# Kernel optimization log

Measured on AMD Instinct MI355X. Metric: run time of the kernel, lower is better.

Reference implementation:

```python
import jax, jax.numpy as jnp
import numpy as np
from jax import lax

B, R, F = 100, 15, 4096       # batch, regions, feature dim
V, E, D, A, T = 10000, 1024, 1024, 512, 500  # vocab, embed, decoder, attention, topic
LIN = 1024                    # autoencoder linear output width
NT = 5                        # sentences per paragraph
L = 52                        # max caption length


def setup_inputs() -> dict:
    key = jax.random.key(0)
    ks = jax.random.split(key, 16)
    g = lambda i, shp, s: jax.random.normal(ks[i], shp, jnp.float32) * s
    return {
        "image_features": g(0, (B, R, F), 1.0),
        "encoded_captions": jax.random.randint(ks[1], (B, NT, L), 0, V),
        "caption_lengths": jax.random.randint(ks[2], (B, NT), 1, L),
        # autoencoder
        "W_lt": g(3, (LIN, F), 0.02), "b_lt": jnp.zeros((LIN,), jnp.float32),
        "conv_w": g(4, (6, 1, 15, 26), 0.05), "conv_b": jnp.zeros((6,), jnp.float32),
        # attention MLP (weight_norm linears == plain linears mathematically)
        "W_feat": g(5, (A, F), 0.02), "b_feat": jnp.zeros((A,), jnp.float32),
        "W_dec": g(6, (A, D), 0.02), "b_dec": jnp.zeros((A,), jnp.float32),
        "W_top": g(7, (A, T), 0.02), "b_top": jnp.zeros((A,), jnp.float32),
        "W_full": g(8, (1, A), 0.02), "b_full": jnp.zeros((1,), jnp.float32),
        # embedding + LSTM cells + output heads
        "emb": g(9, (V, E), 0.1),
        "W_ih1": g(10, (4 * D, E + F + D), 0.01), "W_hh1": g(11, (4 * D, D), 0.01),
        "b_ih1": jnp.zeros((4 * D,), jnp.float32), "b_hh1": jnp.zeros((4 * D,), jnp.float32),
        "W_ih2": g(12, (4 * D, F + D), 0.01), "W_hh2": g(13, (4 * D, D), 0.01),
        "b_ih2": jnp.zeros((4 * D,), jnp.float32), "b_hh2": jnp.zeros((4 * D,), jnp.float32),
        "W_fc1": g(14, (V, D), 0.02), "b_fc1": jnp.zeros((V,), jnp.float32),
        "W_fc": g(15, (V, D), 0.02), "b_fc": jnp.zeros((V,), jnp.float32),
    }


def _lstm_cell(x, h, c, W_ih, W_hh, b_ih, b_hh):
    gates = x @ W_ih.T + b_ih + h @ W_hh.T + b_hh
    i, f, g_, o = jnp.split(gates, 4, axis=-1)
    c = jax.nn.sigmoid(f) * c + jax.nn.sigmoid(i) * jnp.tanh(g_)
    h = jax.nn.sigmoid(o) * jnp.tanh(c)
    return h, c


def reference(image_features, encoded_captions, caption_lengths, W_lt, b_lt,
              conv_w, conv_b, W_feat, b_feat, W_dec, b_dec, W_top, b_top,
              W_full, b_full, emb, W_ih1, W_hh1, b_ih1, b_hh1,
              W_ih2, W_hh2, b_ih2, b_hh2, W_fc1, b_fc1, W_fc, b_fc):
    def per_sample(img, caps, lens):
        # img (R,F), caps (NT,L) int, lens (NT,) int
        img_mean = img.mean(0)  # (F,)
        # autoencoder: linear 4096->1024, conv2d(1->6, k=(15,26), stride 2)
        x = (img @ W_lt.T + b_lt)[None, None]  # (1,1,R,LIN)
        conv = lax.conv_general_dilated(x, conv_w, (2, 2), "VALID",
                                        dimension_numbers=("NCHW", "OIHW", "NCHW"))
        topics = conv[0, :, 0, :] + conv_b[:, None]  # (6, T=500)
        att1 = img @ W_feat.T + b_feat               # (R,A), precomputed once
        # last word of each sentence: caps[t, lens[t]-1]
        last_words = jnp.take_along_axis(caps, (lens - 1)[:, None], axis=1)[:, 0]  # (NT,)
        last_embs = emb[last_words]                  # (NT,E)

        def step(carry, tup):
            h1, c1, h2, c2 = carry
            topic_t, emb_t = tup
            # top-down attention LSTM: cat([h2, img_mean, word_emb])
            x1 = jnp.concatenate([h2, img_mean, emb_t])
            h1, c1 = _lstm_cell(x1, h1, c1, W_ih1, W_hh1, b_ih1, b_hh1)
            # attention over R regions (dropout is identity in eval)
            att = jax.nn.relu(att1 + (h1 @ W_dec.T + b_dec) + (topic_t @ W_top.T + b_top))
            scores = att @ W_full[0] + b_full[0]     # (R,)
            alpha = jax.nn.softmax(scores)
            awe = alpha @ img                        # (F,)
            preds1 = h1 @ W_fc1.T + b_fc1            # (V,)
            h2, c2 = _lstm_cell(jnp.concatenate([awe, h1]), h2, c2,
                                W_ih2, W_hh2, b_ih2, b_hh2)
            preds = h2 @ W_fc.T + b_fc               # (V,)
            return (h1, c1, h2, c2), (preds, preds1)

        z = jnp.zeros((D,), img.dtype)
        _, (preds, preds1) = lax.scan(step, (z, z, z, z), (topics[:NT], last_embs))
        return preds, preds1                          # (NT,V) each

    preds, preds1 = jax.vmap(per_sample)(image_features, encoded_captions, caption_lengths)
    return preds, preds1, encoded_captions, caption_lengths - 1
```

## Files before the change

kernel.cpp:

```cpp
#include <hip/hip_runtime.h>

typedef __attribute__((ext_vector_type(8))) short short8;
typedef __attribute__((ext_vector_type(4))) short short4v;
typedef __attribute__((ext_vector_type(4))) float f32x4;

__device__ __forceinline__ unsigned short f2bf(float f) {
  unsigned int u = __float_as_uint(f);
  u += 0x7fffu + ((u >> 16) & 1u);
  return (unsigned short)(u >> 16);
}
__device__ __forceinline__ float bf2f(unsigned short u) {
  return __uint_as_float(((unsigned int)u) << 16);
}
__device__ __forceinline__ float sigm(float x) { return 1.f / (1.f + expf(-x)); }

template<int NKC>
__global__ __launch_bounds__(256) void gemm_v5(
    const unsigned short* __restrict__ X, int ldx,
    const unsigned short* __restrict__ W, int ldw, int N,
    unsigned short* __restrict__ C, long long slotStride)
{
  __shared__ short8 lds[3584];
  const int tid = threadIdx.x;
  const int lane = tid & 63, wv = tid >> 6;
  const int l16 = lane & 15, kg = (lane >> 4) * 8;
  const int mbase = blockIdx.y * 112;
  const int ncol = blockIdx.x * 64 + wv * 16 + l16;
  const int nrow = (ncol < N) ? ncol : (N - 1);
  const long long k0 = (long long)blockIdx.z * (NKC * 256);
  C += (long long)blockIdx.z * slotStride;

  const unsigned short* wp = W + (size_t)nrow * ldw + kg + k0;
  const unsigned short* xb = X + (size_t)(mbase + l16) * ldx + kg + k0;
  const size_t xrow = (size_t)16 * ldx;

  f32x4 acc[7];
#pragma unroll
  for (int i = 0; i < 7; ++i) acc[i] = (f32x4){0.f, 0.f, 0.f, 0.f};

  for (int kc = 0; kc < NKC; ++kc) {
    if (kc) __syncthreads();
    short8 wbuf[8];
#pragma unroll
    for (int ks = 0; ks < 8; ++ks)
      wbuf[ks] = *(const short8*)(wp + kc * 256 + ks * 32);
    short8 xst[14];
#pragma unroll
    for (int i = 0; i < 14; ++i) {
      const int f = wv + i * 4, mt = f >> 3, ks = f & 7;
      xst[i] = *(const short8*)(xb + (size_t)mt * xrow + kc * 256 + ks * 32);
    }
#pragma unroll
    for (int i = 0; i < 14; ++i) lds[(wv + i * 4) * 64 + lane] = xst[i];
    __syncthreads();
#pragma unroll
    for (int ks = 0; ks < 8; ++ks)
#pragma unroll
      for (int mt = 0; mt < 7; ++mt) {
        short8 a = lds[(mt * 8 + ks) * 64 + lane];
        acc[mt] = __builtin_amdgcn_mfma_f32_16x16x32_bf16(a, wbuf[ks], acc[mt], 0, 0, 0);
      }
  }
  if (ncol < N) {
    const int r0 = (lane >> 4) * 4;
#pragma unroll
    for (int mt = 0; mt < 7; ++mt)
#pragma unroll
      for (int r = 0; r < 4; ++r)
        C[(size_t)(mbase + mt * 16 + r0 + r) * N + ncol] = f2bf(acc[mt][r]);
  }
}

template<int NKC>
__global__ __launch_bounds__(256) void gemm_v5f(
    const unsigned short* __restrict__ X, int ldx,
    const float* __restrict__ W, int ldw, int N,
    unsigned short* __restrict__ C, long long slotStride)
{
  __shared__ short8 lds[3584];
  const int tid = threadIdx.x;
  const int lane = tid & 63, wv = tid >> 6;
  const int l16 = lane & 15, kg = (lane >> 4) * 8;
  const int mbase = blockIdx.y * 112;
  const int ncol = blockIdx.x * 64 + wv * 16 + l16;
  const int nrow = (ncol < N) ? ncol : (N - 1);
  const long long k0 = (long long)blockIdx.z * (NKC * 256);
  C += (long long)blockIdx.z * slotStride;

  const float* wp = W + (size_t)nrow * ldw + kg + k0;
  const unsigned short* xb = X + (size_t)(mbase + l16) * ldx + kg + k0;
  const size_t xrow = (size_t)16 * ldx;

  f32x4 acc[7];
#pragma unroll
  for (int i = 0; i < 7; ++i) acc[i] = (f32x4){0.f, 0.f, 0.f, 0.f};

  for (int kc = 0; kc < NKC; ++kc) {
    if (kc) __syncthreads();
    float4 wa[8], wb[8];
#pragma unroll
    for (int ks = 0; ks < 8; ++ks) {
      wa[ks] = *(const float4*)(wp + kc * 256 + ks * 32);
      wb[ks] = *(const float4*)(wp + kc * 256 + ks * 32 + 4);
    }
    short8 xst[14];
#pragma unroll
    for (int i = 0; i < 14; ++i) {
      const int f = wv + i * 4, mt = f >> 3, ks = f & 7;
      xst[i] = *(const short8*)(xb + (size_t)mt * xrow + kc * 256 + ks * 32);
    }
#pragma unroll
    for (int i = 0; i < 14; ++i) lds[(wv + i * 4) * 64 + lane] = xst[i];
    __syncthreads();
#pragma unroll
    for (int ks = 0; ks < 8; ++ks) {
      short8 w;
      w[0] = (short)f2bf(wa[ks].x); w[1] = (short)f2bf(wa[ks].y);
      w[2] = (short)f2bf(wa[ks].z); w[3] = (short)f2bf(wa[ks].w);
      w[4] = (short)f2bf(wb[ks].x); w[5] = (short)f2bf(wb[ks].y);
      w[6] = (short)f2bf(wb[ks].z); w[7] = (short)f2bf(wb[ks].w);
#pragma unroll
      for (int mt = 0; mt < 7; ++mt) {
        short8 a = lds[(mt * 8 + ks) * 64 + lane];
        acc[mt] = __builtin_amdgcn_mfma_f32_16x16x32_bf16(a, w, acc[mt], 0, 0, 0);
      }
    }
  }
  if (ncol < N) {
    const int r0 = (lane >> 4) * 4;
#pragma unroll
    for (int mt = 0; mt < 7; ++mt)
#pragma unroll
      for (int r = 0; r < 4; ++r)
        C[(size_t)(mbase + mt * 16 + r0 + r) * N + ncol] = f2bf(acc[mt][r]);
  }
}

__global__ __launch_bounds__(256) void k_pack_all(
    const float* __restrict__ Wih1, const float* __restrict__ Whh1,
    const float* __restrict__ Wih2, const float* __restrict__ Whh2,
    const float* __restrict__ Wfc1, const float* __restrict__ Wdec,
    const float* __restrict__ Wfc,  const float* __restrict__ Wtop,
    unsigned short* __restrict__ Wg1, unsigned short* __restrict__ Wg2,
    unsigned short* __restrict__ Wcat, unsigned short* __restrict__ Wfcb,
    unsigned short* __restrict__ Wtopb)
{
  const int i0 = blockIdx.x * 2048 + threadIdx.x;
#pragma unroll
  for (int u = 0; u < 8; ++u) {
    const int i = i0 + u * 256;
    float4 v; unsigned short* dst; long long di;
    if (i < 2097152) {
      int row = i >> 9, c4 = i & 511;
      const float* s = (c4 < 256) ? Wih1 + (size_t)row * 6144 + c4 * 4
                                  : Whh1 + (size_t)row * 1024 + (c4 - 256) * 4;
      v = *(const float4*)s; dst = Wg1; di = i;
    } else if (i < 8388608) {
      int j = i - 2097152; int row = j / 1536, c4 = j - row * 1536;
      const float* s = (c4 < 1280) ? Wih2 + (size_t)row * 5120 + c4 * 4
                                   : Whh2 + (size_t)row * 1024 + (c4 - 1280) * 4;
      v = *(const float4*)s; dst = Wg2; di = j;
    } else if (i < 11079680) {
      int j = i - 8388608; int row = j >> 8, c4 = j & 255;
      const float* s = (row < 10000) ? Wfc1 + (size_t)row * 1024 + c4 * 4
                                     : Wdec + (size_t)(row - 10000) * 1024 + c4 * 4;
      v = *(const float4*)s; dst = Wcat; di = j;
    } else if (i < 13639680) { int j = i - 11079680; v = ((const float4*)Wfc)[j]; dst = Wfcb; di = j; }
    else {
      int j = i - 13639680; if (j >= 65536) continue;
      int n = j >> 7, c4 = j & 127;
      v = (c4 < 125) ? *(const float4*)(Wtop + (size_t)n * 500 + c4 * 4)
                     : (float4){0.f, 0.f, 0.f, 0.f};
      dst = Wtopb; di = j;
    }
    short4v o; o[0] = (short)f2bf(v.x); o[1] = (short)f2bf(v.y);
    o[2] = (short)f2bf(v.z); o[3] = (short)f2bf(v.w);
    ((short4v*)dst)[di] = o;
  }
}

__global__ __launch_bounds__(256) void k_ximg2(const float* __restrict__ img,
    unsigned short* __restrict__ Ximg, unsigned short* __restrict__ Xmean) {
  int idx = blockIdx.x * 256 + threadIdx.x;
  int b = idx >> 10, f4 = idx & 1023;
  float4 s = {0.f, 0.f, 0.f, 0.f};
#pragma unroll
  for (int r = 0; r < 15; ++r) {
    float4 v = *(const float4*)(img + (((size_t)(b * 15 + r)) << 12) + f4 * 4);
    s.x += v.x; s.y += v.y; s.z += v.z; s.w += v.w;
    short4v o; o[0] = (short)f2bf(v.x); o[1] = (short)f2bf(v.y);
    o[2] = (short)f2bf(v.z); o[3] = (short)f2bf(v.w);
    *(short4v*)(Ximg + (((size_t)(b * 15 + r)) << 12) + f4 * 4) = o;
  }
  short4v m; m[0] = (short)f2bf(s.x * (1.f / 15.f)); m[1] = (short)f2bf(s.y * (1.f / 15.f));
  m[2] = (short)f2bf(s.z * (1.f / 15.f)); m[3] = (short)f2bf(s.w * (1.f / 15.f));
  *(short4v*)(Xmean + (((size_t)b) << 12) + f4 * 4) = m;
}

__global__ __launch_bounds__(256) void k_reduce(const unsigned short* __restrict__ P,
    long long ss, int nslots, const float* __restrict__ bias, int colmask,
    float* __restrict__ out, int total) {
  int idx = blockIdx.x * 256 + threadIdx.x;
  if (idx >= total) return;
  float s = bias ? bias[idx & colmask] : 0.f;
  for (int sl = 0; sl < nslots; ++sl) s += bf2f(P[(size_t)sl * ss + idx]);
  out[idx] = s;
}

__global__ __launch_bounds__(512) void k_conv(const unsigned short* __restrict__ px,
    const float* __restrict__ blt, const float* __restrict__ cw,
    const float* __restrict__ cb, unsigned short* __restrict__ Xtop) {
  int b = blockIdx.x;
  __shared__ float L[15 * 1024];
  for (int i = threadIdx.x; i < 15 * 1024; i += 512) {
    float s = blt[i & 1023];
#pragma unroll
    for (int sl = 0; sl < 8; ++sl)
      s += bf2f(px[(size_t)sl * 1605632 + (size_t)b * 15360 + i]);
    L[i] = s;
  }
  __syncthreads();
  for (int idx = threadIdx.x; idx < 2500; idx += 512) {
    int tt = idx / 500, w = idx - tt * 500;
    float s = cb[tt];
    for (int kh = 0; kh < 15; ++kh) {
      const float* lr = &L[kh * 1024 + 2 * w];
      const float* wr = &cw[(tt * 15 + kh) * 26];
#pragma unroll
      for (int kw = 0; kw < 26; ++kw) s += lr[kw] * wr[kw];
    }
    Xtop[((size_t)(b * 5 + tt)) * 512 + w] = f2bf(s);
  }
}

__global__ __launch_bounds__(256) void k_gw(const int* __restrict__ caps,
    const int* __restrict__ lens, const float* __restrict__ emb,
    unsigned short* __restrict__ Xemb, float* __restrict__ out2,
    float* __restrict__ out3) {
  int idx = blockIdx.x * 256 + threadIdx.x;
  int bt = idx >> 10, e = idx & 1023;
  if (bt < 500) {
    int w = caps[bt * 52 + lens[bt] - 1];
    Xemb[idx] = f2bf(emb[(size_t)w * 1024 + e]);
  } else if (bt < 560) Xemb[idx] = 0;
  if (idx < 26000) out2[idx] = (float)caps[idx];
  if (idx < 500) out3[idx] = (float)(lens[idx] - 1);
}

__global__ __launch_bounds__(256) void k_gbase1(const unsigned short* __restrict__ P,
    const float* __restrict__ bih, const float* __restrict__ bhh,
    float* __restrict__ gb) {
  int idx = blockIdx.x * 256 + threadIdx.x;
  int m = idx >> 12, n = idx & 4095;
  float s = bih[n] + bhh[n];
#pragma unroll
  for (int sl = 0; sl < 8; ++sl) s += bf2f(P[((size_t)sl * 112 + m) * 4096 + n]);
  gb[idx] = s;
}

__global__ __launch_bounds__(256) void k_lstm1(const unsigned short* __restrict__ P,
    const float* __restrict__ gb1, const float* __restrict__ gemb, int t,
    float* __restrict__ c1, unsigned short* __restrict__ Xh1,
    unsigned short* __restrict__ X1, unsigned short* __restrict__ X2) {
  int idx = blockIdx.x * 256 + threadIdx.x;
  int b = idx >> 10, j = idx & 1023;
  float g[4];
#pragma unroll
  for (int x = 0; x < 4; ++x) {
    int col = (x << 10) + j;
    float s = gb1[b * 4096 + col] + gemb[((size_t)b * 5 + t) * 4096 + col];
#pragma unroll
    for (int sl = 0; sl < 8; ++sl) s += bf2f(P[((size_t)sl * 112 + b) * 4096 + col]);
    g[x] = s;
  }
  float c = sigm(g[1]) * c1[idx] + sigm(g[0]) * tanhf(g[2]);
  float h = sigm(g[3]) * tanhf(c);
  c1[idx] = c;
  unsigned short hb = f2bf(h);
  Xh1[idx] = hb;
  X1[b * 2048 + 1024 + j] = hb;
  X2[(size_t)b * 6144 + 4096 + j] = hb;
}

__global__ __launch_bounds__(256) void k_attpred(const float* __restrict__ att1,
    const unsigned short* __restrict__ px, const float* __restrict__ bdec,
    const float* __restrict__ btop, const unsigned short* __restrict__ ttopb,
    const float* __restrict__ wfull, int t,
    const unsigned short* __restrict__ Ximg, unsigned short* __restrict__ X2,
    const float* __restrict__ bfc1, float* __restrict__ outp) {
  if (blockIdx.x >= 100) {
    int idx = (blockIdx.x - 100) * 256 + threadIdx.x;
    if (idx >= 250000) return;
    int b = idx / 2500, v4 = (idx - b * 2500) * 4;
    float4 bv = *(const float4*)(bfc1 + v4);
    short4v p0 = *(const short4v*)(px + (size_t)b * 10512 + v4);
    short4v p1 = *(const short4v*)(px + (size_t)(112 + b) * 10512 + v4);
    short4v p2 = *(const short4v*)(px + (size_t)(224 + b) * 10512 + v4);
    short4v p3 = *(const short4v*)(px + (size_t)(336 + b) * 10512 + v4);
    float4 o;
    o.x = bv.x + bf2f(p0[0]) + bf2f(p1[0]) + bf2f(p2[0]) + bf2f(p3[0]);
    o.y = bv.y + bf2f(p0[1]) + bf2f(p1[1]) + bf2f(p2[1]) + bf2f(p3[1]);
    o.z = bv.z + bf2f(p0[2]) + bf2f(p1[2]) + bf2f(p2[2]) + bf2f(p3[2]);
    o.w = bv.w + bf2f(p0[3]) + bf2f(p1[3]) + bf2f(p2[3]) + bf2f(p3[3]);
    *(float4*)(outp + ((size_t)b * 5 + t) * 10000 + v4) = o;
    return;
  }
  int b = blockIdx.x;
  int tid = threadIdx.x;
  int r = tid & 15, ch = tid >> 4;
  __shared__ float sp[16][17];
  __shared__ float al[16];
  float s = 0.f;
  if (r < 15) {
    const float* a1 = att1 + ((size_t)b * 15 + r) * 512;
    const unsigned short* tp = ttopb + ((size_t)b * 5 + t) * 512;
#pragma unroll
    for (int j = 0; j < 32; ++j) {
      int n = ch * 32 + j;
      float ad = bdec[n] + btop[n]
               + bf2f(px[((size_t)0 * 112 + b) * 10512 + 10000 + n])
               + bf2f(px[((size_t)1 * 112 + b) * 10512 + 10000 + n])
               + bf2f(px[((size_t)2 * 112 + b) * 10512 + 10000 + n])
               + bf2f(px[((size_t)3 * 112 + b) * 10512 + 10000 + n]);
      float v = a1[n] + ad + bf2f(tp[n]);
      s += fmaxf(v, 0.f) * wfull[n];
    }
  }
  sp[r][ch] = s;
  __syncthreads();
  if (tid == 0) {
    float sc[15];
    float m = -1e30f;
    for (int rr = 0; rr < 15; ++rr) {
      float x = 0.f;
      for (int cc = 0; cc < 16; ++cc) x += sp[rr][cc];
      sc[rr] = x; m = fmaxf(m, x);
    }
    float sum = 0.f;
    for (int rr = 0; rr < 15; ++rr) { sc[rr] = expf(sc[rr] - m); sum += sc[rr]; }
    float inv = 1.f / sum;
    for (int rr = 0; rr < 15; ++rr) al[rr] = sc[rr] * inv;
  }
  __syncthreads();
  for (int f = tid; f < 4096; f += 256) {
    float s2 = 0.f;
#pragma unroll
    for (int rr = 0; rr < 15; ++rr)
      s2 += al[rr] * bf2f(Ximg[((size_t)b * 15 + rr) * 4096 + f]);
    X2[(size_t)b * 6144 + f] = f2bf(s2);
  }
}

__global__ __launch_bounds__(256) void k_lstm2(const unsigned short* __restrict__ P,
    const float* __restrict__ bih, const float* __restrict__ bhh,
    float* __restrict__ c2, unsigned short* __restrict__ Xh2,
    unsigned short* __restrict__ X1, unsigned short* __restrict__ X2) {
  int idx = blockIdx.x * 256 + threadIdx.x;
  int b = idx >> 10, j = idx & 1023;
  float g[4];
#pragma unroll
  for (int x = 0; x < 4; ++x) {
    int col = (x << 10) + j;
    float s = bih[col] + bhh[col];
#pragma unroll
    for (int sl = 0; sl < 12; ++sl) s += bf2f(P[((size_t)sl * 112 + b) * 4096 + col]);
    g[x] = s;
  }
  float c = sigm(g[1]) * c2[idx] + sigm(g[0]) * tanhf(g[2]);
  float h = sigm(g[3]) * tanhf(c);
  c2[idx] = c;
  unsigned short hb = f2bf(h);
  Xh2[idx] = hb;
  X1[b * 2048 + j] = hb;
  X2[(size_t)b * 6144 + 5120 + j] = hb;
}

__global__ __launch_bounds__(256) void k_eppred(const unsigned short* __restrict__ P,
    const float* __restrict__ bias, float* __restrict__ outp, int t) {
  int idx = blockIdx.x * 256 + threadIdx.x;
  if (idx >= 250000) return;
  int b = idx / 2500, v4 = (idx - b * 2500) * 4;
  float4 bv = *(const float4*)(bias + v4);
  short4v p0 = *(const short4v*)(P + (size_t)b * 10000 + v4);
  short4v p1 = *(const short4v*)(P + (size_t)(112 + b) * 10000 + v4);
  short4v p2 = *(const short4v*)(P + (size_t)(224 + b) * 10000 + v4);
  short4v p3 = *(const short4v*)(P + (size_t)(336 + b) * 10000 + v4);
  float4 o;
  o.x = bv.x + bf2f(p0[0]) + bf2f(p1[0]) + bf2f(p2[0]) + bf2f(p3[0]);
  o.y = bv.y + bf2f(p0[1]) + bf2f(p1[1]) + bf2f(p2[1]) + bf2f(p3[1]);
  o.z = bv.z + bf2f(p0[2]) + bf2f(p1[2]) + bf2f(p2[2]) + bf2f(p3[2]);
  o.w = bv.w + bf2f(p0[3]) + bf2f(p1[3]) + bf2f(p2[3]) + bf2f(p3[3]);
  *(float4*)(outp + ((size_t)b * 5 + t) * 10000 + v4) = o;
}

extern "C" void kernel_launch(void* const* d_in, const int* in_sizes, int n_in,
                              void* d_out, int out_size, void* d_ws, size_t ws_size,
                              hipStream_t stream) {
  (void)in_sizes; (void)n_in; (void)out_size;
  const float* imgf  = (const float*)d_in[0];
  const int*   caps  = (const int*)d_in[1];
  const int*   lens  = (const int*)d_in[2];
  const float* W_lt  = (const float*)d_in[3];
  const float* b_lt  = (const float*)d_in[4];
  const float* convw = (const float*)d_in[5];
  const float* convb = (const float*)d_in[6];
  const float* W_feat = (const float*)d_in[7];
  const float* b_feat = (const float*)d_in[8];
  const float* W_dec = (const float*)d_in[9];
  const float* b_dec = (const float*)d_in[10];
  const float* W_top = (const float*)d_in[11];
  const float* b_top = (const float*)d_in[12];
  const float* W_full = (const float*)d_in[13];
  const float* b_full = (const float*)d_in[14];  (void)b_full;
  const float* emb   = (const float*)d_in[15];
  const float* W_ih1 = (const float*)d_in[16];
  const float* W_hh1 = (const float*)d_in[17];
  const float* b_ih1 = (const float*)d_in[18];
  const float* b_hh1 = (const float*)d_in[19];
  const float* W_ih2 = (const float*)d_in[20];
  const float* W_hh2 = (const float*)d_in[21];
  const float* b_ih2 = (const float*)d_in[22];
  const float* b_hh2 = (const float*)d_in[23];
  const float* W_fc1 = (const float*)d_in[24];
  const float* b_fc1 = (const float*)d_in[25];
  const float* W_fc  = (const float*)d_in[26];
  const float* b_fc  = (const float*)d_in[27];
  float* out = (float*)d_out;

  char* ws = (char*)d_ws;
  size_t off = 0;
  auto alloc = [&](size_t bytes) -> size_t {
    size_t o = off; off = (off + bytes + 255) & ~(size_t)255; return o;
  };
  const size_t oZERO  = off;
  const size_t oXimg  = alloc(1568ull * 4096 * 2);
  const size_t oXmean = alloc(112ull * 4096 * 2);
  const size_t oX1    = alloc(112ull * 2048 * 2);
  const size_t oX2    = alloc(112ull * 6144 * 2);
  const size_t oXh1   = alloc(112ull * 1024 * 2);
  const size_t oXh2   = alloc(112ull * 1024 * 2);
  const size_t oc1    = alloc(100ull * 1024 * 4);
  const size_t oc2    = alloc(100ull * 1024 * 4);
  const size_t oXtop  = alloc(560ull * 512 * 2);
  const size_t zeroBytes = off - oZERO;
  const size_t oXemb  = alloc(560ull * 1024 * 2);
  const size_t oTtopb = alloc(560ull * 512 * 2);
  const size_t oatt1  = alloc(1568ull * 512 * 4);
  const size_t ogb1   = alloc(112ull * 4096 * 4);
  const size_t ogemb  = alloc(560ull * 4096 * 4);
  const size_t opg    = alloc(12ull * 112 * 4096 * 2);
  const size_t opx    = alloc(8ull * 1568 * 1024 * 2);
  const size_t opp    = alloc(4ull * 112 * 10000 * 2);
  const size_t oWg1   = alloc(4096ull * 2048 * 2);
  const size_t oWg2   = alloc(4096ull * 6144 * 2);
  const size_t oWcat  = alloc(10512ull * 1024 * 2);
  const size_t oWfcb  = alloc(10000ull * 1024 * 2);
  const size_t oWtopb = alloc(512ull * 512 * 2);
  if (ws_size < off) return;

  unsigned short* Ximg  = (unsigned short*)(ws + oXimg);
  unsigned short* Xmean = (unsigned short*)(ws + oXmean);
  unsigned short* Xemb  = (unsigned short*)(ws + oXemb);
  unsigned short* X1    = (unsigned short*)(ws + oX1);
  unsigned short* X2    = (unsigned short*)(ws + oX2);
  unsigned short* Xh1   = (unsigned short*)(ws + oXh1);
  unsigned short* Xh2   = (unsigned short*)(ws + oXh2);
  float* c1    = (float*)(ws + oc1);
  float* c2    = (float*)(ws + oc2);
  unsigned short* Xtop  = (unsigned short*)(ws + oXtop);
  unsigned short* Ttopb = (unsigned short*)(ws + oTtopb);
  float* att1  = (float*)(ws + oatt1);
  float* gb1   = (float*)(ws + ogb1);
  float* gemb  = (float*)(ws + ogemb);
  unsigned short* pg    = (unsigned short*)(ws + opg);
  unsigned short* px    = (unsigned short*)(ws + opx);
  unsigned short* pp    = (unsigned short*)(ws + opp);
  unsigned short* Wg1   = (unsigned short*)(ws + oWg1);
  unsigned short* Wg2   = (unsigned short*)(ws + oWg2);
  unsigned short* Wcat  = (unsigned short*)(ws + oWcat);
  unsigned short* Wfcb  = (unsigned short*)(ws + oWfcb);
  unsigned short* Wtopb = (unsigned short*)(ws + oWtopb);

  const long long S4  = 112ll * 4096;
  const long long SP1 = 112ll * 10512;
  const long long SP  = 112ll * 10000;

  hipMemsetAsync(ws + oZERO, 0, zeroBytes, stream);

  k_ximg2<<<400, 256, 0, stream>>>(imgf, Ximg, Xmean);
  k_pack_all<<<6692, 256, 0, stream>>>(W_ih1, W_hh1, W_ih2, W_hh2, W_fc1, W_dec,
                                       W_fc, W_top, Wg1, Wg2, Wcat, Wfcb, Wtopb);
  gemm_v5f<2><<<dim3(16, 14, 8), 256, 0, stream>>>(Ximg, 4096, W_lt, 4096, 1024,
                                                   px, 1568ll * 1024);
  k_conv<<<100, 512, 0, stream>>>(px, b_lt, convw, convb, Xtop);
  gemm_v5<2><<<dim3(8, 5, 1), 256, 0, stream>>>(Xtop, 512, Wtopb, 512, 512, Ttopb, 0);
  gemm_v5f<2><<<dim3(8, 14, 8), 256, 0, stream>>>(Ximg, 4096, W_feat, 4096, 512,
                                                  px, 1568ll * 512);
  k_reduce<<<3136, 256, 0, stream>>>(px, 1568ll * 512, 8, b_feat, 511, att1, 1568 * 512);
  k_gw<<<2240, 256, 0, stream>>>(caps, lens, emb, Xemb, out + 10000000, out + 10026000);
  gemm_v5f<2><<<dim3(64, 1, 8), 256, 0, stream>>>(Xmean, 4096, W_ih1 + 1024, 6144, 4096,
                                                  pg, S4);
  k_gbase1<<<1792, 256, 0, stream>>>(pg, b_ih1, b_hh1, gb1);
  gemm_v5f<1><<<dim3(64, 5, 4), 256, 0, stream>>>(Xemb, 1024, W_ih1 + 5120, 6144, 4096,
                                                  px, 560ll * 4096);
  k_reduce<<<8960, 256, 0, stream>>>(px, 560ll * 4096, 4, nullptr, 4095, gemb, 560 * 4096);

  for (int t = 0; t < 5; ++t) {
    gemm_v5<1><<<dim3(64, 1, 8), 256, 0, stream>>>(X1, 2048, Wg1, 2048, 4096, pg, S4);
    k_lstm1<<<400, 256, 0, stream>>>(pg, gb1, gemb, t, c1, Xh1, X1, X2);
    gemm_v5<1><<<dim3(165, 1, 4), 256, 0, stream>>>(Xh1, 1024, Wcat, 1024, 10512, px, SP1);
    k_attpred<<<1077, 256, 0, stream>>>(att1, px, b_dec, b_top, Ttopb, W_full, t,
                                        Ximg, X2, b_fc1, out + 5000000);
    gemm_v5<2><<<dim3(64, 1, 12), 256, 0, stream>>>(X2, 6144, Wg2, 6144, 4096, pg, S4);
    k_lstm2<<<400, 256, 0, stream>>>(pg, b_ih2, b_hh2, c2, Xh2, X1, X2);
    gemm_v5<1><<<dim3(157, 1, 4), 256, 0, stream>>>(Xh2, 1024, Wfcb, 1024, 10000, pp, SP);
    k_eppred<<<977, 256, 0, stream>>>(pp, b_fc, out, t);
  }
}
```

Baseline: 697.5 us.

## Merge independent kernels into combined launches and defer output-head GEMM across steps

Collapses the prologue into fewer kernels. One prep kernel now does image conversion, embedding gather and weight packing, and one multi-GEMM kernel runs the four setup GEMMs. The emb GEMM now runs without split-K and writes fp32 directly. In the time loop, the fc-output GEMM for step t-1 is fused into the same launch as the step t gate GEMM, and its reduction is fused with the LSTM1 epilogue, with a tail launch for the last step. The aim is fewer launches and more blocks in flight per launch. The cost is heterogeneous blocks per launch and a larger LDS/register footprint in the shared core.

```diff
diff --git a/kernel.cpp b/kernel.cpp
--- a/kernel.cpp
+++ b/kernel.cpp
@@ -14,36 +14,47 @@
 }
 __device__ __forceinline__ float sigm(float x) { return 1.f / (1.f + expf(-x)); }
 
-template<int NKC>
-__global__ __launch_bounds__(256) void gemm_v5(
+template<int NKC, bool WF32, bool OUTF32>
+__device__ __forceinline__ void gemm_core(
     const unsigned short* __restrict__ X, int ldx,
-    const unsigned short* __restrict__ W, int ldw, int N,
-    unsigned short* __restrict__ C, long long slotStride)
-{
-  __shared__ short8 lds[3584];
+    const void* __restrict__ Wv, int ldw, int N,
+    void* __restrict__ Cv, long long slotStride,
+    const float* __restrict__ bias, long long ldc, int rowLim,
+    int bx, int by, int bz, short8* lds)
+{
   const int tid = threadIdx.x;
   const int lane = tid & 63, wv = tid >> 6;
   const int l16 = lane & 15, kg = (lane >> 4) * 8;
-  const int mbase = blockIdx.y * 112;
-  const int ncol = blockIdx.x * 64 + wv * 16 + l16;
+  const int mbase = by * 112;
+  const int ncol = bx * 64 + wv * 16 + l16;
   const int nrow = (ncol < N) ? ncol : (N - 1);
-  const long long k0 = (long long)blockIdx.z * (NKC * 256);
-  C += (long long)blockIdx.z * slotStride;
-
-  const unsigned short* wp = W + (size_t)nrow * ldw + kg + k0;
+  const long long k0 = (long long)bz * (NKC * 256);
+
   const unsigned short* xb = X + (size_t)(mbase + l16) * ldx + kg + k0;
   const size_t xrow = (size_t)16 * ldx;
+  const unsigned short* wpb = (const unsigned short*)Wv + (size_t)nrow * ldw + kg + k0;
+  const float* wpf = (const float*)Wv + (size_t)nrow * ldw + kg + k0;
 
   f32x4 acc[7];
 #pragma unroll
   for (int i = 0; i < 7; ++i) acc[i] = (f32x4){0.f, 0.f, 0.f, 0.f};
 
+#pragma unroll
   for (int kc = 0; kc < NKC; ++kc) {
     if (kc) __syncthreads();
     short8 wbuf[8];
-#pragma unroll
-    for (int ks = 0; ks < 8; ++ks)
-      wbuf[ks] = *(const short8*)(wp + kc * 256 + ks * 32);
+    float4 wa[8], wb[8];
+    if constexpr (WF32) {
+#pragma unroll
+      for (int ks = 0; ks < 8; ++ks) {
+        wa[ks] = *(const float4*)(wpf + kc * 256 + ks * 32);
+        wb[ks] = *(const float4*)(wpf + kc * 256 + ks * 32 + 4);
+      }
+    } else {
+#pragma unroll
+      for (int ks = 0; ks < 8; ++ks)
+        wbuf[ks] = *(const short8*)(wpb + kc * 256 + ks * 32);
+    }
     short8 xst[14];
 #pragma unroll
     for (int i = 0; i < 14; ++i) {
@@ -54,71 +65,16 @@
     for (int i = 0; i < 14; ++i) lds[(wv + i * 4) * 64 + lane] = xst[i];
     __syncthreads();
 #pragma unroll
-    for (int ks = 0; ks < 8; ++ks)
-#pragma unroll
-      for (int mt = 0; mt < 7; ++mt) {
-        short8 a = lds[(mt * 8 + ks) * 64 + lane];
-        acc[mt] = __builtin_amdgcn_mfma_f32_16x16x32_bf16(a, wbuf[ks], acc[mt], 0, 0, 0);
-      }
-  }
-  if (ncol < N) {
-    const int r0 = (lane >> 4) * 4;
-#pragma unroll
-    for (int mt = 0; mt < 7; ++mt)
-#pragma unroll
-      for (int r = 0; r < 4; ++r)
-        C[(size_t)(mbase + mt * 16 + r0 + r) * N + ncol] = f2bf(acc[mt][r]);
-  }
-}
-
-template<int NKC>
-__global__ __launch_bounds__(256) void gemm_v5f(
-    const unsigned short* __restrict__ X, int ldx,
-    const float* __restrict__ W, int ldw, int N,
-    unsigned short* __restrict__ C, long long slotStride)
-{
-  __shared__ short8 lds[3584];
-  const int tid = threadIdx.x;
-  const int lane = tid & 63, wv = tid >> 6;
-  const int l16 = lane & 15, kg = (lane >> 4) * 8;
-  const int mbase = blockIdx.y * 112;
-  const int ncol = blockIdx.x * 64 + wv * 16 + l16;
-  const int nrow = (ncol < N) ? ncol : (N - 1);
-  const long long k0 = (long long)blockIdx.z * (NKC * 256);
-  C += (long long)blockIdx.z * slotStride;
-
-  const float* wp = W + (size_t)nrow * ldw + kg + k0;
-  const unsigned short* xb = X + (size_t)(mbase + l16) * ldx + kg + k0;
-  const size_t xrow = (size_t)16 * ldx;
-
-  f32x4 acc[7];
-#pragma unroll
-  for (int i = 0; i < 7; ++i) acc[i] = (f32x4){0.f, 0.f, 0.f, 0.f};
-
-  for (int kc = 0; kc < NKC; ++kc) {
-    if (kc) __syncthreads();
-    float4 wa[8], wb[8];
-#pragma unroll
-    for (int ks = 0; ks < 8; ++ks) {
-      wa[ks] = *(const float4*)(wp + kc * 256 + ks * 32);
-      wb[ks] = *(const float4*)(wp + kc * 256 + ks * 32 + 4);
-    }
-    short8 xst[14];
-#pragma unroll
-    for (int i = 0; i < 14; ++i) {
-      const int f = wv + i * 4, mt = f >> 3, ks = f & 7;
-      xst[i] = *(const short8*)(xb + (size_t)mt * xrow + kc * 256 + ks * 32);
-    }
-#pragma unroll
-    for (int i = 0; i < 14; ++i) lds[(wv + i * 4) * 64 + lane] = xst[i];
-    __syncthreads();
-#pragma unroll
     for (int ks = 0; ks < 8; ++ks) {
       short8 w;
-      w[0] = (short)f2bf(wa[ks].x); w[1] = (short)f2bf(wa[ks].y);
-      w[2] = (short)f2bf(wa[ks].z); w[3] = (short)f2bf(wa[ks].w);
-      w[4] = (short)f2bf(wb[ks].x); w[5] = (short)f2bf(wb[ks].y);
-      w[6] = (short)f2bf(wb[ks].z); w[7] = (short)f2bf(wb[ks].w);
+      if constexpr (WF32) {
+        w[0] = (short)f2bf(wa[ks].x); w[1] = (short)f2bf(wa[ks].y);
+        w[2] = (short)f2bf(wa[ks].z); w[3] = (short)f2bf(wa[ks].w);
+        w[4] = (short)f2bf(wb[ks].x); w[5] = (short)f2bf(wb[ks].y);
+        w[6] = (short)f2bf(wb[ks].z); w[7] = (short)f2bf(wb[ks].w);
+      } else {
+        w = wbuf[ks];
+      }
 #pragma unroll
       for (int mt = 0; mt < 7; ++mt) {
         short8 a = lds[(mt * 8 + ks) * 64 + lane];
@@ -128,91 +84,163 @@
   }
   if (ncol < N) {
     const int r0 = (lane >> 4) * 4;
-#pragma unroll
-    for (int mt = 0; mt < 7; ++mt)
-#pragma unroll
-      for (int r = 0; r < 4; ++r)
-        C[(size_t)(mbase + mt * 16 + r0 + r) * N + ncol] = f2bf(acc[mt][r]);
-  }
-}
-
-__global__ __launch_bounds__(256) void k_pack_all(
+    if constexpr (OUTF32) {
+      float* outF = (float*)Cv;
+      const float bv = bias ? bias[ncol] : 0.f;
+#pragma unroll
+      for (int mt = 0; mt < 7; ++mt)
+#pragma unroll
+        for (int r = 0; r < 4; ++r) {
+          const int row = mbase + mt * 16 + r0 + r;
+          if (row < rowLim) outF[(size_t)row * ldc + ncol] = acc[mt][r] + bv;
+        }
+    } else {
+      unsigned short* C = (unsigned short*)Cv + (long long)bz * slotStride;
+#pragma unroll
+      for (int mt = 0; mt < 7; ++mt)
+#pragma unroll
+        for (int r = 0; r < 4; ++r)
+          C[(size_t)(mbase + mt * 16 + r0 + r) * N + ncol] = f2bf(acc[mt][r]);
+    }
+  }
+}
+
+template<int NKC>
+__global__ __launch_bounds__(256) void gemm_bb(
+    const unsigned short* __restrict__ X, int ldx,
+    const unsigned short* __restrict__ W, int ldw, int N,
+    unsigned short* __restrict__ C, long long ss)
+{
+  __shared__ short8 lds[3584];
+  gemm_core<NKC, false, false>(X, ldx, W, ldw, N, C, ss, nullptr, 0, 0,
+                               blockIdx.x, blockIdx.y, blockIdx.z, lds);
+}
+
+__global__ __launch_bounds__(256) void k_prep(
+    const float* __restrict__ img, const int* __restrict__ caps,
+    const int* __restrict__ lens, const float* __restrict__ emb,
     const float* __restrict__ Wih1, const float* __restrict__ Whh1,
     const float* __restrict__ Wih2, const float* __restrict__ Whh2,
     const float* __restrict__ Wfc1, const float* __restrict__ Wdec,
     const float* __restrict__ Wfc,  const float* __restrict__ Wtop,
+    unsigned short* __restrict__ Ximg, unsigned short* __restrict__ Xmean,
+    unsigned short* __restrict__ Xemb, float* __restrict__ out2,
+    float* __restrict__ out3,
     unsigned short* __restrict__ Wg1, unsigned short* __restrict__ Wg2,
     unsigned short* __restrict__ Wcat, unsigned short* __restrict__ Wfcb,
     unsigned short* __restrict__ Wtopb)
 {
-  const int i0 = blockIdx.x * 2048 + threadIdx.x;
-#pragma unroll
-  for (int u = 0; u < 8; ++u) {
-    const int i = i0 + u * 256;
-    float4 v; unsigned short* dst; long long di;
-    if (i < 2097152) {
-      int row = i >> 9, c4 = i & 511;
-      const float* s = (c4 < 256) ? Wih1 + (size_t)row * 6144 + c4 * 4
-                                  : Whh1 + (size_t)row * 1024 + (c4 - 256) * 4;
-      v = *(const float4*)s; dst = Wg1; di = i;
-    } else if (i < 8388608) {
-      int j = i - 2097152; int row = j / 1536, c4 = j - row * 1536;
-      const float* s = (c4 < 1280) ? Wih2 + (size_t)row * 5120 + c4 * 4
-                                   : Whh2 + (size_t)row * 1024 + (c4 - 1280) * 4;
-      v = *(const float4*)s; dst = Wg2; di = j;
-    } else if (i < 11079680) {
-      int j = i - 8388608; int row = j >> 8, c4 = j & 255;
-      const float* s = (row < 10000) ? Wfc1 + (size_t)row * 1024 + c4 * 4
-                                     : Wdec + (size_t)(row - 10000) * 1024 + c4 * 4;
-      v = *(const float4*)s; dst = Wcat; di = j;
-    } else if (i < 13639680) { int j = i - 11079680; v = ((const float4*)Wfc)[j]; dst = Wfcb; di = j; }
-    else {
-      int j = i - 13639680; if (j >= 65536) continue;
-      int n = j >> 7, c4 = j & 127;
-      v = (c4 < 125) ? *(const float4*)(Wtop + (size_t)n * 500 + c4 * 4)
-                     : (float4){0.f, 0.f, 0.f, 0.f};
-      dst = Wtopb; di = j;
-    }
-    short4v o; o[0] = (short)f2bf(v.x); o[1] = (short)f2bf(v.y);
-    o[2] = (short)f2bf(v.z); o[3] = (short)f2bf(v.w);
-    ((short4v*)dst)[di] = o;
-  }
-}
-
-__global__ __launch_bounds__(256) void k_ximg2(const float* __restrict__ img,
-    unsigned short* __restrict__ Ximg, unsigned short* __restrict__ Xmean) {
-  int idx = blockIdx.x * 256 + threadIdx.x;
-  int b = idx >> 10, f4 = idx & 1023;
-  float4 s = {0.f, 0.f, 0.f, 0.f};
-#pragma unroll
-  for (int r = 0; r < 15; ++r) {
-    float4 v = *(const float4*)(img + (((size_t)(b * 15 + r)) << 12) + f4 * 4);
-    s.x += v.x; s.y += v.y; s.z += v.z; s.w += v.w;
-    short4v o; o[0] = (short)f2bf(v.x); o[1] = (short)f2bf(v.y);
-    o[2] = (short)f2bf(v.z); o[3] = (short)f2bf(v.w);
-    *(short4v*)(Ximg + (((size_t)(b * 15 + r)) << 12) + f4 * 4) = o;
-  }
-  short4v m; m[0] = (short)f2bf(s.x * (1.f / 15.f)); m[1] = (short)f2bf(s.y * (1.f / 15.f));
-  m[2] = (short)f2bf(s.z * (1.f / 15.f)); m[3] = (short)f2bf(s.w * (1.f / 15.f));
-  *(short4v*)(Xmean + (((size_t)b) << 12) + f4 * 4) = m;
-}
-
-__global__ __launch_bounds__(256) void k_reduce(const unsigned short* __restrict__ P,
-    long long ss, int nslots, const float* __restrict__ bias, int colmask,
-    float* __restrict__ out, int total) {
-  int idx = blockIdx.x * 256 + threadIdx.x;
-  if (idx >= total) return;
-  float s = bias ? bias[idx & colmask] : 0.f;
-  for (int sl = 0; sl < nslots; ++sl) s += bf2f(P[(size_t)sl * ss + idx]);
-  out[idx] = s;
-}
-
-__global__ __launch_bounds__(512) void k_conv(const unsigned short* __restrict__ px,
-    const float* __restrict__ blt, const float* __restrict__ cw,
-    const float* __restrict__ cb, unsigned short* __restrict__ Xtop) {
+  const int bid = blockIdx.x, tid = threadIdx.x;
+  if (bid < 400) {
+    int idx = bid * 256 + tid;
+    int b = idx >> 10, f4 = idx & 1023;
+    float4 s = {0.f, 0.f, 0.f, 0.f};
+#pragma unroll
+    for (int r = 0; r < 15; ++r) {
+      float4 v = *(const float4*)(img + (((size_t)(b * 15 + r)) << 12) + f4 * 4);
+      s.x += v.x; s.y += v.y; s.z += v.z; s.w += v.w;
+      short4v o; o[0] = (short)f2bf(v.x); o[1] = (short)f2bf(v.y);
+      o[2] = (short)f2bf(v.z); o[3] = (short)f2bf(v.w);
+      *(short4v*)(Ximg + (((size_t)(b * 15 + r)) << 12) + f4 * 4) = o;
+    }
+    short4v m;
+    m[0] = (short)f2bf(s.x * (1.f / 15.f)); m[1] = (short)f2bf(s.y * (1.f / 15.f));
+    m[2] = (short)f2bf(s.z * (1.f / 15.f)); m[3] = (short)f2bf(s.w * (1.f / 15.f));
+    *(short4v*)(Xmean + (((size_t)b) << 12) + f4 * 4) = m;
+    return;
+  }
+  if (bid < 2640) {
+    int idx = (bid - 400) * 256 + tid;
+    int bt = idx >> 10, e = idx & 1023;
+    if (bt < 500) {
+      int w = caps[bt * 52 + lens[bt] - 1];
+      Xemb[idx] = f2bf(emb[(size_t)w * 1024 + e]);
+    } else if (bt < 560) Xemb[idx] = 0;
+    if (idx < 26000) out2[idx] = (float)caps[idx];
+    if (idx < 500) out3[idx] = (float)(lens[idx] - 1);
+    return;
+  }
+  int i = (bid - 2640) * 256 + tid;
+  float4 v; unsigned short* dst; long long di;
+  if (i < 2097152) {
+    int row = i >> 9, c4 = i & 511;
+    const float* s = (c4 < 256) ? Wih1 + (size_t)row * 6144 + c4 * 4
+                                : Whh1 + (size_t)row * 1024 + (c4 - 256) * 4;
+    v = *(const float4*)s; dst = Wg1; di = i;
+  } else if (i < 8388608) {
+    int j = i - 2097152; int row = j / 1536, c4 = j - row * 1536;
+    const float* s = (c4 < 1280) ? Wih2 + (size_t)row * 5120 + c4 * 4
+                                 : Whh2 + (size_t)row * 1024 + (c4 - 1280) * 4;
+    v = *(const float4*)s; dst = Wg2; di = j;
+  } else if (i < 11079680) {
+    int j = i - 8388608; int row = j >> 8, c4 = j & 255;
+    const float* s = (row < 10000) ? Wfc1 + (size_t)row * 1024 + c4 * 4
+                                   : Wdec + (size_t)(row - 10000) * 1024 + c4 * 4;
+    v = *(const float4*)s; dst = Wcat; di = j;
+  } else if (i < 13639680) { int j = i - 11079680; v = ((const float4*)Wfc)[j]; dst = Wfcb; di = j; }
+  else {
+    int j = i - 13639680; if (j >= 65536) return;
+    int n = j >> 7, c4 = j & 127;
+    v = (c4 < 125) ? *(const float4*)(Wtop + (size_t)n * 500 + c4 * 4)
+                   : (float4){0.f, 0.f, 0.f, 0.f};
+    dst = Wtopb; di = j;
+  }
+  short4v o; o[0] = (short)f2bf(v.x); o[1] = (short)f2bf(v.y);
+  o[2] = (short)f2bf(v.z); o[3] = (short)f2bf(v.w);
+  ((short4v*)dst)[di] = o;
+}
+
+__global__ __launch_bounds__(256) void k_gemmA(
+    const unsigned short* __restrict__ Ximg, const unsigned short* __restrict__ Xmean,
+    const unsigned short* __restrict__ Xemb,
+    const float* __restrict__ Wlt, const float* __restrict__ Wft,
+    const float* __restrict__ Wih1,
+    unsigned short* __restrict__ px, unsigned short* __restrict__ pax,
+    unsigned short* __restrict__ pg, float* __restrict__ gemb)
+{
+  __shared__ short8 lds[3584];
+  const int id = blockIdx.x;
+  if (id < 1792) {
+    int bx = id & 15, r = id >> 4, by = r % 14, bz = r / 14;
+    gemm_core<2, true, false>(Ximg, 4096, Wlt, 4096, 1024, px, 1568ll * 1024,
+                              nullptr, 0, 0, bx, by, bz, lds);
+  } else if (id < 2688) {
+    int i = id - 1792;
+    int bx = i & 7, r = i >> 3, by = r % 14, bz = r / 14;
+    gemm_core<2, true, false>(Ximg, 4096, Wft, 4096, 512, pax, 1568ll * 512,
+                              nullptr, 0, 0, bx, by, bz, lds);
+  } else if (id < 3200) {
+    int i = id - 2688;
+    int bx = i & 63, bz = i >> 6;
+    gemm_core<2, true, false>(Xmean, 4096, Wih1 + 1024, 6144, 4096, pg,
+                              112ll * 4096, nullptr, 0, 0, bx, 0, bz, lds);
+  } else {
+    int i = id - 3200;
+    int bx = i & 63, by = i >> 6;
+    gemm_core<4, true, true>(Xemb, 1024, Wih1 + 5120, 6144, 4096, gemb, 0,
+                             nullptr, 4096, 560, bx, by, 0, lds);
+  }
+}
+
+__global__ __launch_bounds__(256) void k_convred(
+    const unsigned short* __restrict__ px, const float* __restrict__ blt,
+    const float* __restrict__ cw, const float* __restrict__ cb,
+    unsigned short* __restrict__ Xtop,
+    const unsigned short* __restrict__ pax, const float* __restrict__ bfeat,
+    float* __restrict__ att1)
+{
+  if (blockIdx.x >= 100) {
+    int idx = (blockIdx.x - 100) * 256 + threadIdx.x;
+    if (idx >= 1568 * 512) return;
+    float s = bfeat[idx & 511];
+#pragma unroll
+    for (int sl = 0; sl < 8; ++sl) s += bf2f(pax[(size_t)sl * 802816 + idx]);
+    att1[idx] = s;
+    return;
+  }
   int b = blockIdx.x;
   __shared__ float L[15 * 1024];
-  for (int i = threadIdx.x; i < 15 * 1024; i += 512) {
+  for (int i = threadIdx.x; i < 15 * 1024; i += 256) {
     float s = blt[i & 1023];
 #pragma unroll
     for (int sl = 0; sl < 8; ++sl)
@@ -220,7 +248,7 @@
     L[i] = s;
   }
   __syncthreads();
-  for (int idx = threadIdx.x; idx < 2500; idx += 512) {
+  for (int idx = threadIdx.x; idx < 2500; idx += 256) {
     int tt = idx / 500, w = idx - tt * 500;
     float s = cb[tt];
     for (int kh = 0; kh < 15; ++kh) {
@@ -233,35 +261,72 @@
   }
 }
 
-__global__ __launch_bounds__(256) void k_gw(const int* __restrict__ caps,
-    const int* __restrict__ lens, const float* __restrict__ emb,
-    unsigned short* __restrict__ Xemb, float* __restrict__ out2,
-    float* __restrict__ out3) {
-  int idx = blockIdx.x * 256 + threadIdx.x;
-  int bt = idx >> 10, e = idx & 1023;
-  if (bt < 500) {
-    int w = caps[bt * 52 + lens[bt] - 1];
-    Xemb[idx] = f2bf(emb[(size_t)w * 1024 + e]);
-  } else if (bt < 560) Xemb[idx] = 0;
-  if (idx < 26000) out2[idx] = (float)caps[idx];
-  if (idx < 500) out3[idx] = (float)(lens[idx] - 1);
-}
-
-__global__ __launch_bounds__(256) void k_gbase1(const unsigned short* __restrict__ P,
-    const float* __restrict__ bih, const float* __restrict__ bhh,
-    float* __restrict__ gb) {
-  int idx = blockIdx.x * 256 + threadIdx.x;
+__global__ __launch_bounds__(256) void k_misc(
+    const unsigned short* __restrict__ Xtop, const unsigned short* __restrict__ Wtopb,
+    unsigned short* __restrict__ Ttopb,
+    const unsigned short* __restrict__ pg, const float* __restrict__ bih,
+    const float* __restrict__ bhh, float* __restrict__ gb)
+{
+  __shared__ short8 lds[3584];
+  if (blockIdx.x < 40) {
+    int bx = blockIdx.x & 7, by = blockIdx.x >> 3;
+    gemm_core<2, false, false>(Xtop, 512, Wtopb, 512, 512, Ttopb, 0,
+                               nullptr, 0, 0, bx, by, 0, lds);
+    return;
+  }
+  int idx = (blockIdx.x - 40) * 256 + threadIdx.x;
+  if (idx >= 112 * 4096) return;
   int m = idx >> 12, n = idx & 4095;
   float s = bih[n] + bhh[n];
 #pragma unroll
-  for (int sl = 0; sl < 8; ++sl) s += bf2f(P[((size_t)sl * 112 + m) * 4096 + n]);
+  for (int sl = 0; sl < 8; ++sl) s += bf2f(pg[((size_t)sl * 112 + m) * 4096 + n]);
   gb[idx] = s;
 }
 
-__global__ __launch_bounds__(256) void k_lstm1(const unsigned short* __restrict__ P,
-    const float* __restrict__ gb1, const float* __restrict__ gemb, int t,
-    float* __restrict__ c1, unsigned short* __restrict__ Xh1,
-    unsigned short* __restrict__ X1, unsigned short* __restrict__ X2) {
+__global__ __launch_bounds__(256) void k_g1preds(
+    const unsigned short* __restrict__ X1, const unsigned short* __restrict__ Wg1,
+    unsigned short* __restrict__ pg,
+    const unsigned short* __restrict__ Xh2, const unsigned short* __restrict__ Wfcb,
+    unsigned short* __restrict__ pp)
+{
+  __shared__ short8 lds[3584];
+  if (blockIdx.x < 512) {
+    int bx = blockIdx.x & 63, bz = blockIdx.x >> 6;
+    gemm_core<1, false, false>(X1, 2048, Wg1, 2048, 4096, pg, 112ll * 4096,
+                               nullptr, 0, 0, bx, 0, bz, lds);
+  } else {
+    int i = blockIdx.x - 512;
+    int bx = i % 157, bz = i / 157;
+    gemm_core<1, false, false>(Xh2, 1024, Wfcb, 1024, 10000, pp, 112ll * 10000,
+                               nullptr, 0, 0, bx, 0, bz, lds);
+  }
+}
+
+__global__ __launch_bounds__(256) void k_lstm1ep(
+    const unsigned short* __restrict__ P, const float* __restrict__ gb1,
+    const float* __restrict__ gemb, int t, float* __restrict__ c1,
+    unsigned short* __restrict__ Xh1, unsigned short* __restrict__ X1,
+    unsigned short* __restrict__ X2,
+    const unsigned short* __restrict__ pp, const float* __restrict__ bfc,
+    float* __restrict__ out0)
+{
+  if (blockIdx.x >= 400) {
+    int idx = (blockIdx.x - 400) * 256 + threadIdx.x;
+    if (idx >= 250000) return;
+    int b = idx / 2500, v4 = (idx - b * 2500) * 4;
+    float4 bv = *(const float4*)(bfc + v4);
+    short4v p0 = *(const short4v*)(pp + (size_t)b * 10000 + v4);
+    short4v p1 = *(const short4v*)(pp + (size_t)(112 + b) * 10000 + v4);
+    short4v p2 = *(const short4v*)(pp + (size_t)(224 + b) * 10000 + v4);
+    short4v p3 = *(const short4v*)(pp + (size_t)(336 + b) * 10000 + v4);
+    float4 o;
+    o.x = bv.x + bf2f(p0[0]) + bf2f(p1[0]) + bf2f(p2[0]) + bf2f(p3[0]);
+    o.y = bv.y + bf2f(p0[1]) + bf2f(p1[1]) + bf2f(p2[1]) + bf2f(p3[1]);
+    o.z = bv.z + bf2f(p0[2]) + bf2f(p1[2]) + bf2f(p2[2]) + bf2f(p3[2]);
+    o.w = bv.w + bf2f(p0[3]) + bf2f(p1[3]) + bf2f(p2[3]) + bf2f(p3[3]);
+    *(float4*)(out0 + ((size_t)b * 5 + (t - 1)) * 10000 + v4) = o;
+    return;
+  }
   int idx = blockIdx.x * 256 + threadIdx.x;
   int b = idx >> 10, j = idx & 1023;
   float g[4];
@@ -450,6 +515,7 @@
   const size_t ogemb  = alloc(560ull * 4096 * 4);
   const size_t opg    = alloc(12ull * 112 * 4096 * 2);
   const size_t opx    = alloc(8ull * 1568 * 1024 * 2);
+  const size_t opax   = alloc(8ull * 1568 * 512 * 2);
   const size_t opp    = alloc(4ull * 112 * 10000 * 2);
   const size_t oWg1   = alloc(4096ull * 2048 * 2);
   const size_t oWg2   = alloc(4096ull * 6144 * 2);
@@ -474,6 +540,7 @@
   float* gemb  = (float*)(ws + ogemb);
   unsigned short* pg    = (unsigned short*)(ws + opg);
   unsigned short* px    = (unsigned short*)(ws + opx);
+  unsigned short* pax   = (unsigned short*)(ws + opax);
   unsigned short* pp    = (unsigned short*)(ws + opp);
   unsigned short* Wg1   = (unsigned short*)(ws + oWg1);
   unsigned short* Wg2   = (unsigned short*)(ws + oWg2);
@@ -483,37 +550,31 @@
 
   const long long S4  = 112ll * 4096;
   const long long SP1 = 112ll * 10512;
-  const long long SP  = 112ll * 10000;
 
   hipMemsetAsync(ws + oZERO, 0, zeroBytes, stream);
 
-  k_ximg2<<<400, 256, 0, stream>>>(imgf, Ximg, Xmean);
-  k_pack_all<<<6692, 256, 0, stream>>>(W_ih1, W_hh1, W_ih2, W_hh2, W_fc1, W_dec,
-                                       W_fc, W_top, Wg1, Wg2, Wcat, Wfcb, Wtopb);
-  gemm_v5f<2><<<dim3(16, 14, 8), 256, 0, stream>>>(Ximg, 4096, W_lt, 4096, 1024,
-                                                   px, 1568ll * 1024);
-  k_conv<<<100, 512, 0, stream>>>(px, b_lt, convw, convb, Xtop);
-  gemm_v5<2><<<dim3(8, 5, 1), 256, 0, stream>>>(Xtop, 512, Wtopb, 512, 512, Ttopb, 0);
-  gemm_v5f<2><<<dim3(8, 14, 8), 256, 0, stream>>>(Ximg, 4096, W_feat, 4096, 512,
-                                                  px, 1568ll * 512);
-  k_reduce<<<3136, 256, 0, stream>>>(px, 1568ll * 512, 8, b_feat, 511, att1, 1568 * 512);
-  k_gw<<<2240, 256, 0, stream>>>(caps, lens, emb, Xemb, out + 10000000, out + 10026000);
-  gemm_v5f<2><<<dim3(64, 1, 8), 256, 0, stream>>>(Xmean, 4096, W_ih1 + 1024, 6144, 4096,
-                                                  pg, S4);
-  k_gbase1<<<1792, 256, 0, stream>>>(pg, b_ih1, b_hh1, gb1);
-  gemm_v5f<1><<<dim3(64, 5, 4), 256, 0, stream>>>(Xemb, 1024, W_ih1 + 5120, 6144, 4096,
-                                                  px, 560ll * 4096);
-  k_reduce<<<8960, 256, 0, stream>>>(px, 560ll * 4096, 4, nullptr, 4095, gemb, 560 * 4096);
+  k_prep<<<56176, 256, 0, stream>>>(imgf, caps, lens, emb,
+      W_ih1, W_hh1, W_ih2, W_hh2, W_fc1, W_dec, W_fc, W_top,
+      Ximg, Xmean, Xemb, out + 10000000, out + 10026000,
+      Wg1, Wg2, Wcat, Wfcb, Wtopb);
+  k_gemmA<<<3520, 256, 0, stream>>>(Ximg, Xmean, Xemb, W_lt, W_feat, W_ih1,
+                                    px, pax, pg, gemb);
+  k_convred<<<3236, 256, 0, stream>>>(px, b_lt, convw, convb, Xtop,
+                                      pax, b_feat, att1);
+  k_misc<<<1832, 256, 0, stream>>>(Xtop, Wtopb, Ttopb, pg, b_ih1, b_hh1, gb1);
 
   for (int t = 0; t < 5; ++t) {
-    gemm_v5<1><<<dim3(64, 1, 8), 256, 0, stream>>>(X1, 2048, Wg1, 2048, 4096, pg, S4);
-    k_lstm1<<<400, 256, 0, stream>>>(pg, gb1, gemb, t, c1, Xh1, X1, X2);
-    gemm_v5<1><<<dim3(165, 1, 4), 256, 0, stream>>>(Xh1, 1024, Wcat, 1024, 10512, px, SP1);
+    k_g1preds<<<(t == 0 ? 512 : 1140), 256, 0, stream>>>(X1, Wg1, pg, Xh2, Wfcb, pp);
+    k_lstm1ep<<<(t == 0 ? 400 : 1377), 256, 0, stream>>>(pg, gb1, gemb, t, c1,
+                                                         Xh1, X1, X2, pp, b_fc, out);
+    gemm_bb<1><<<dim3(165, 1, 4), 256, 0, stream>>>(Xh1, 1024, Wcat, 1024, 10512,
+                                                    px, SP1);
     k_attpred<<<1077, 256, 0, stream>>>(att1, px, b_dec, b_top, Ttopb, W_full, t,
                                         Ximg, X2, b_fc1, out + 5000000);
-    gemm_v5<2><<<dim3(64, 1, 12), 256, 0, stream>>>(X2, 6144, Wg2, 6144, 4096, pg, S4);
+    gemm_bb<2><<<dim3(64, 1, 12), 256, 0, stream>>>(X2, 6144, Wg2, 6144, 4096, pg, S4);
     k_lstm2<<<400, 256, 0, stream>>>(pg, b_ih2, b_hh2, c2, Xh2, X1, X2);
-    gemm_v5<1><<<dim3(157, 1, 4), 256, 0, stream>>>(Xh2, 1024, Wfcb, 1024, 10000, pp, SP);
-    k_eppred<<<977, 256, 0, stream>>>(pp, b_fc, out, t);
-  }
-}
+  }
+  gemm_bb<1><<<dim3(157, 1, 4), 256, 0, stream>>>(Xh2, 1024, Wfcb, 1024, 10000,
+                                                  pp, 112ll * 10000);
+  k_eppred<<<977, 256, 0, stream>>>(pp, b_fc, out, 4);
+}
```

New measurement: 712.4 us. +2.1%, slower.
